# Optimization experiments

Hardware: AMD Instinct MI355X
Metric: run time of the kernel (lower is better)

The kernel has to match this reference:

```python
import jax, jax.numpy as jnp
import numpy as np

B, H, W, C = 32, 128, 128, 64
MX, MY = 32, 32  # modes_x, modes_y


def setup_inputs() -> dict:
    key = jax.random.key(0)
    k1, k2, k3, k4 = jax.random.split(key, 4)
    # glorot-ish scales for the spectral and conv weights
    wscale = (2.0 / (C + C)) ** 0.5
    return {
        "x": jax.random.normal(k1, (B, H, W, C), dtype=jnp.float32),
        "w_real": jax.random.normal(k2, (MX, MY, C, C), dtype=jnp.float32) * wscale,
        "w_imag": jax.random.normal(k3, (MX, MY, C, C), dtype=jnp.float32) * wscale,
        "conv_w": jax.random.normal(k4, (C, C), dtype=jnp.float32) * wscale,
        "conv_b": jnp.zeros((C,), dtype=jnp.float32),
    }


def reference(x, w_real, w_imag, conv_w, conv_b):
    # Complex spectral mixing weights [MX, MY, Cin, Cout]
    weights = jax.lax.complex(w_real, w_imag)
    # tf.signal.fft2d transforms the innermost TWO axes of [B,H,W,C],
    # i.e. axes (W, C); jnp.fft.fft2 default axes=(-2,-1) matches exactly.
    x_ft = jnp.fft.fft2(x.astype(jnp.complex64))           # [B,H,W,C] complex64
    # Mode truncation on axes (H, W), as in the original code.
    x_ft_trunc = x_ft[:, :MX, :MY, :]                      # [B,MX,MY,C]
    # Complex channel-mixing einsum over the low modes.
    x_ft_proc = jnp.einsum('bxyi,xyio->bxyo', x_ft_trunc, weights)  # [B,MX,MY,C]
    # Zero-pad back to the full grid on (H, W).
    x_ft_padded = jnp.pad(x_ft_proc,
                          ((0, 0), (0, H - MX), (0, W - MY), (0, 0)))
    # IFFT again over innermost two axes (W, C), take real part.
    x_spec = jnp.real(jnp.fft.ifft2(x_ft_padded))          # [B,H,W,C] float32
    # 1x1 conv (pointwise channel mix) + bias on the raw input.
    x_local = jnp.einsum('bhwi,io->bhwo', x, conv_w) + conv_b
    return jax.nn.relu(x_spec + x_local)
```

## Files before the change

kernel.cpp:

```cpp
#include <hip/hip_runtime.h>

typedef __attribute__((ext_vector_type(8))) short short8;
typedef __attribute__((ext_vector_type(4))) short bf16x4;
typedef __attribute__((ext_vector_type(4))) float f32x4;
typedef unsigned short ushort_t;

#define MFMA(a, b, c) __builtin_amdgcn_mfma_f32_16x16x32_bf16((a), (b), (c), 0, 0, 0)

constexpr int NB = 32, NHt = 128, NWd = 128, NC = 64, MX = 32;
constexpr float TWO_PI = 6.28318530717958647692f;

constexpr size_t TAB_T3 = 32768;
constexpr size_t TAB_T4 = 49152;
constexpr size_t XY_OFF = 65536;

__device__ inline ushort_t f2bf(float f) {
    union { float f; unsigned int u; } v; v.f = f;
    unsigned int r = v.u + 0x7FFFu + ((v.u >> 16) & 1u);
    return (ushort_t)(r >> 16);
}
__device__ inline int sxor(int row) { return ((row >> 3) & 3) << 4; }

__global__ __launch_bounds__(512) void k1_fwd(
    const float* __restrict__ x, char* __restrict__ tabs, ushort_t* __restrict__ XY)
{
    const int b = blockIdx.x, h = blockIdx.y;
    const int tid = threadIdx.x, lane = tid & 63, wv = tid >> 6;
    constexpr int SXT  = 0;
    constexpr int M1RE = 17408;
    constexpr int M1IM = 17408 + 4608;
    __shared__ __align__(16) char sm[26624];

    if (b == 0 && h == 0) {
        {
            int nt2 = tid >> 7, ks2 = (tid >> 6) & 1, l = tid & 63;
            int cc2 = (l & 15) + 16 * nt2, ob = (l >> 4) * 8 + 32 * ks2;
            short8 vre, vim;
            #pragma unroll
            for (int j = 0; j < 8; ++j) {
                float a = (float)(((ob + j) * cc2) & 63) * (TWO_PI / 64.f);
                float s, c; __sincosf(a, &s, &c);
                vre[j] = (short)f2bf(c); vim[j] = (short)f2bf(s);
            }
            *reinterpret_cast<short8*>(tabs + TAB_T3 + tid * 32)      = vre;
            *reinterpret_cast<short8*>(tabs + TAB_T3 + tid * 32 + 16) = vim;
        }
        {
            int mt2 = tid >> 6, l = tid & 63;
            int w = (l & 15) + 16 * mt2, ub = (l >> 4) * 8;
            short8 vre, vim;
            #pragma unroll
            for (int j = 0; j < 8; ++j) {
                float a = (float)((w * (ub + j)) & 127) * (TWO_PI / 128.f);
                float s, c; __sincosf(a, &s, &c);
                vre[j] = (short)f2bf(c * 0.0001220703125f);
                vim[j] = (short)f2bf(s * 0.0001220703125f);
            }
            *reinterpret_cast<short8*>(tabs + TAB_T4 + tid * 32)      = vre;
            *reinterpret_cast<short8*>(tabs + TAB_T4 + tid * 32 + 16) = vim;
        }
    }

    const float* xs = x + ((size_t)(b * NHt + h)) * (NWd * NC);
    #pragma unroll
    for (int i = 0; i < 4; ++i) {
        int idx = tid + 512 * i;
        int w = idx >> 4, c4 = (idx & 15) * 4;
        f32x4 v = *reinterpret_cast<const f32x4*>(xs + w * 64 + c4);
        #pragma unroll
        for (int j = 0; j < 4; ++j)
            *(ushort_t*)(sm + SXT + (c4 + j) * 272 + ((w * 2) ^ sxor(c4 + j))) = f2bf(v[j]);
    }
    __syncthreads();

    const int mt = wv >> 2, nt = wv & 3;
    f32x4 m1r = {0.f,0.f,0.f,0.f}, m1i = {0.f,0.f,0.f,0.f};
    const int cc = (lane & 15) + 16 * nt;
    const int uu = (lane & 15) + 16 * mt;
    #pragma unroll
    for (int ks = 0; ks < 4; ++ks) {
        short8 bfrag = *reinterpret_cast<const short8*>(
            sm + SXT + cc * 272 + (((lane >> 4) * 16 + 64 * ks) ^ sxor(cc)));
        int wb = (lane >> 4) * 8 + 32 * ks;
        short8 are, aim;
        #pragma unroll
        for (int j = 0; j < 8; ++j) {
            float a = (float)((uu * (wb + j)) & 127) * (TWO_PI / 128.f);
            float s, c; __sincosf(a, &s, &c);
            are[j] = (short)f2bf(c); aim[j] = (short)f2bf(-s);
        }
        m1r = MFMA(are, bfrag, m1r);
        m1i = MFMA(aim, bfrag, m1i);
    }
    #pragma unroll
    for (int r = 0; r < 4; ++r) {
        int u = (lane >> 4) * 4 + r + 16 * mt;
        int c = (lane & 15) + 16 * nt;
        *(ushort_t*)(sm + M1RE + u * 144 + c * 2) = f2bf(m1r[r]);
        *(ushort_t*)(sm + M1IM + u * 144 + c * 2) = f2bf(m1i[r]);
    }
    __syncthreads();

    f32x4 xP = {0.f,0.f,0.f,0.f}, xQ = {0.f,0.f,0.f,0.f}, xI = {0.f,0.f,0.f,0.f};
    const int kk = (lane & 15) + 16 * nt;
    #pragma unroll
    for (int ks = 0; ks < 2; ++ks) {
        short8 are = *reinterpret_cast<const short8*>(
            sm + M1RE + ((lane & 15) + 16 * mt) * 144 + (lane >> 4) * 16 + 64 * ks);
        short8 aim = *reinterpret_cast<const short8*>(
            sm + M1IM + ((lane & 15) + 16 * mt) * 144 + (lane >> 4) * 16 + 64 * ks);
        int cb2 = (lane >> 4) * 8 + 32 * ks;
        short8 bre, bim;
        #pragma unroll
        for (int j = 0; j < 8; ++j) {
            float a = (float)((kk * (cb2 + j)) & 63) * (TWO_PI / 64.f);
            float s, c; __sincosf(a, &s, &c);
            bre[j] = (short)f2bf(c); bim[j] = (short)f2bf(-s);
        }
        xP = MFMA(are, bre, xP);
        xQ = MFMA(aim, bim, xQ);
        xI = MFMA(are, bim, xI);
        xI = MFMA(aim, bre, xI);
    }
    #pragma unroll
    for (int r = 0; r < 4; ++r) {
        int u = (lane >> 4) * 4 + r + 16 * mt;
        int k = (lane & 15) + 16 * nt;
        *(ushort_t*)(sm + SXT + 0    + u * 128 + k * 2) = f2bf(xP[r] - xQ[r]);
        *(ushort_t*)(sm + SXT + 4096 + u * 128 + k * 2) = f2bf(xI[r]);
    }
    __syncthreads();

    {
        int u = tid >> 4, comp = (tid >> 3) & 1, k8 = (tid & 7) * 8;
        short8 v = *reinterpret_cast<const short8*>(sm + SXT + comp * 4096 + u * 128 + k8 * 2);
        size_t hu = (size_t)(h * 32 + u);
        *reinterpret_cast<short8*>(XY + ((hu * 2 + comp) * 32 + b) * 64 + k8) = v;
    }
}

__global__ __launch_bounds__(256) void k2_mix(
    const float* __restrict__ wre, const float* __restrict__ wim, ushort_t* __restrict__ XY)
{
    const int h = blockIdx.x, u = blockIdx.y;
    const int tid = threadIdx.x, lane = tid & 63, wv = tid >> 6;
    constexpr int XRE = 0, XIM = 4608, WTR = 9216, WTI = 18432;
    __shared__ __align__(16) char sm[27648];
    const size_t hu = (size_t)(h * 32 + u);

    #pragma unroll
    for (int it = 0; it < 2; ++it) {
        int row = (tid >> 3) + 32 * it;
        int comp = row >> 5, bb = row & 31, k8 = (tid & 7) * 8;
        short8 v = *reinterpret_cast<const short8*>(XY + ((hu * 2 + comp) * 32 + bb) * 64 + k8);
        *reinterpret_cast<short8*>(sm + (comp ? XIM : XRE) + bb * 144 + k8 * 2) = v;
    }
    const float* wr = wre + hu * 4096;
    const float* wi = wim + hu * 4096;
    #pragma unroll
    for (int i = 0; i < 4; ++i) {
        int idx = tid + 256 * i;
        int k = idx >> 4, o4 = (idx & 15) * 4;
        f32x4 vr = __builtin_nontemporal_load(reinterpret_cast<const f32x4*>(wr + k * 64 + o4));
        f32x4 vi = __builtin_nontemporal_load(reinterpret_cast<const f32x4*>(wi + k * 64 + o4));
        #pragma unroll
        for (int j = 0; j < 4; ++j) {
            int o = o4 + j, koff = (k * 2) ^ sxor(o);
            *(ushort_t*)(sm + WTR + o * 144 + koff) = f2bf(vr[j]);
            *(ushort_t*)(sm + WTI + o * 144 + koff) = f2bf(vi[j]);
        }
    }
    __syncthreads();

    const int mt = wv >> 1;
    f32x4 yRe[2], yIm[2];
    #pragma unroll
    for (int half = 0; half < 2; ++half) {
        const int nt = (wv & 1) * 2 + half;
        const int oo = (lane & 15) + 16 * nt;
        f32x4 yP = {0.f,0.f,0.f,0.f}, yQ = {0.f,0.f,0.f,0.f}, yI = {0.f,0.f,0.f,0.f};
        #pragma unroll
        for (int ks = 0; ks < 2; ++ks) {
            int woff = ((lane >> 4) * 16 + 64 * ks) ^ sxor(oo);
            short8 are = *reinterpret_cast<const short8*>(
                sm + XRE + ((lane & 15) + 16 * mt) * 144 + (lane >> 4) * 16 + 64 * ks);
            short8 aim = *reinterpret_cast<const short8*>(
                sm + XIM + ((lane & 15) + 16 * mt) * 144 + (lane >> 4) * 16 + 64 * ks);
            short8 bre = *reinterpret_cast<const short8*>(sm + WTR + oo * 144 + woff);
            short8 bim = *reinterpret_cast<const short8*>(sm + WTI + oo * 144 + woff);
            yP = MFMA(are, bre, yP); yQ = MFMA(aim, bim, yQ);
            yI = MFMA(are, bim, yI); yI = MFMA(aim, bre, yI);
        }
        #pragma unroll
        for (int r = 0; r < 4; ++r) { yRe[half][r] = yP[r] - yQ[r]; yIm[half][r] = yI[r]; }
    }
    __syncthreads();

    #pragma unroll
    for (int half = 0; half < 2; ++half) {
        const int nt = (wv & 1) * 2 + half;
        #pragma unroll
        for (int r = 0; r < 4; ++r) {
            int bb = (lane >> 4) * 4 + r + 16 * mt;
            int o = (lane & 15) + 16 * nt;
            *(ushort_t*)(sm + 0    + bb * 128 + o * 2) = f2bf(yRe[half][r]);
            *(ushort_t*)(sm + 4096 + bb * 128 + o * 2) = f2bf(yIm[half][r]);
        }
    }
    __syncthreads();

    #pragma unroll
    for (int it = 0; it < 2; ++it) {
        int flat = tid + 256 * it;
        short8 v = *reinterpret_cast<const short8*>(sm + flat * 16);
        *reinterpret_cast<short8*>(XY + hu * 4096 + flat * 8) = v;
    }
}

__global__ __launch_bounds__(512, 4) void k3_inv(
    const float* __restrict__ x, const float* __restrict__ cw, const float* __restrict__ cb,
    const char* __restrict__ tabs, const ushort_t* __restrict__ XY, float* __restrict__ out)
{
    const int b = blockIdx.x, h = blockIdx.y;
    const int tid = threadIdx.x, lane = tid & 63, wv = tid >> 6;
    constexpr int ST_RE = 0, ST_IM = 5120;
    constexpr int XB   = 10240;
    constexpr int CWT  = 28672;
    constexpr int SCB  = 37888;
    constexpr int OUTB = 38144;
    constexpr int YRE  = 38144;
    constexpr int YIM  = 38144 + 4608;
    __shared__ __align__(16) char sm[72960];

    const float* xs = x + ((size_t)(b * NHt + h)) * (NWd * NC);
    f32x4 xv[4];
    #pragma unroll
    for (int i = 0; i < 4; ++i) {
        int idx = tid + 512 * i;
        int w = idx >> 4, c4 = (idx & 15) * 4;
        xv[i] = __builtin_nontemporal_load(reinterpret_cast<const f32x4*>(xs + w * 64 + c4));
    }
    short8 yv = {}, gre = {}, gim = {};
    if (h < MX) {
        int u = tid >> 4, comp = (tid >> 3) & 1, o8 = (tid & 7) * 8;
        size_t hu = (size_t)(h * 32 + u);
        yv = *reinterpret_cast<const short8*>(XY + ((hu * 2 + comp) * 32 + b) * 64 + o8);
        const char* t4 = tabs + TAB_T4 + ((wv * 64 + lane) * 32);
        gre = *reinterpret_cast<const short8*>(t4);
        gim = *reinterpret_cast<const short8*>(t4 + 16);
    }

    #pragma unroll
    for (int i = 0; i < 4; ++i) {
        int idx = tid + 512 * i;
        int w = idx >> 4, c4 = (idx & 15) * 4;
        bf16x4 pk = { (short)f2bf(xv[i][0]), (short)f2bf(xv[i][1]),
                      (short)f2bf(xv[i][2]), (short)f2bf(xv[i][3]) };
        *reinterpret_cast<bf16x4*>(sm + XB + w * 144 + c4 * 2) = pk;
    }
    #pragma unroll
    for (int i = 0; i < 2; ++i) {
        int ii = (tid >> 4) + 32 * i;
        #pragma unroll
        for (int j = 0; j < 4; ++j) {
            int o = (tid & 15) + 16 * j;
            *(ushort_t*)(sm + CWT + o * 144 + ii * 2) = f2bf(cw[ii * 64 + o]);
        }
    }
    if (tid < 64) ((float*)(sm + SCB))[tid] = cb[tid];

    if (h < MX) {
        {
            int u = tid >> 4, comp = (tid >> 3) & 1, o8 = (tid & 7) * 8;
            *reinterpret_cast<short8*>(sm + (comp ? YIM : YRE) + u * 144 + o8 * 2) = yv;
        }
        __syncthreads();
        const int mt = wv >> 2, nt = wv & 3;
        f32x4 sP = {0.f,0.f,0.f,0.f}, sQ = {0.f,0.f,0.f,0.f}, sI = {0.f,0.f,0.f,0.f};
        #pragma unroll
        for (int ks = 0; ks < 2; ++ks) {
            short8 are = *reinterpret_cast<const short8*>(
                sm + YRE + ((lane & 15) + 16 * mt) * 144 + (lane >> 4) * 16 + 64 * ks);
            short8 aim = *reinterpret_cast<const short8*>(
                sm + YIM + ((lane & 15) + 16 * mt) * 144 + (lane >> 4) * 16 + 64 * ks);
            const char* t3 = tabs + TAB_T3 + (((nt * 2 + ks) * 64 + lane) * 32);
            short8 bre = *reinterpret_cast<const short8*>(t3);
            short8 bim = *reinterpret_cast<const short8*>(t3 + 16);
            sP = MFMA(are, bre, sP); sQ = MFMA(aim, bim, sQ);
            sI = MFMA(are, bim, sI); sI = MFMA(aim, bre, sI);
        }
        #pragma unroll
        for (int r = 0; r < 4; ++r) {
            int u = (lane >> 4) * 4 + r + 16 * mt;
            int c = (lane & 15) + 16 * nt;
            *(ushort_t*)(sm + ST_RE + c * 80 + u * 2) = f2bf(sP[r] - sQ[r]);
            *(ushort_t*)(sm + ST_IM + c * 80 + u * 2) = f2bf(sI[r]);
        }
    }
    __syncthreads();

    #pragma unroll
    for (int nt = 0; nt < 4; ++nt) {
        f32x4 acc = {0.f,0.f,0.f,0.f};
        #pragma unroll
        for (int ks = 0; ks < 2; ++ks) {
            short8 ah = *reinterpret_cast<const short8*>(
                sm + XB + ((lane & 15) + 16 * wv) * 144 + (lane >> 4) * 16 + 64 * ks);
            short8 bw = *reinterpret_cast<const short8*>(
                sm + CWT + ((lane & 15) + 16 * nt) * 144 + (lane >> 4) * 16 + 64 * ks);
            acc = MFMA(ah, bw, acc);
        }
        f32x4 sp = {0.f,0.f,0.f,0.f}, sq = {0.f,0.f,0.f,0.f};
        if (h < MX) {
            short8 bre = *reinterpret_cast<const short8*>(
                sm + ST_RE + ((lane & 15) + 16 * nt) * 80 + (lane >> 4) * 16);
            short8 bim = *reinterpret_cast<const short8*>(
                sm + ST_IM + ((lane & 15) + 16 * nt) * 80 + (lane >> 4) * 16);
            sp = MFMA(gre, bre, sp);
            sq = MFMA(gim, bim, sq);
        }
        #pragma unroll
        for (int r = 0; r < 4; ++r) {
            int w = (lane >> 4) * 4 + r + 16 * wv;
            int c = (lane & 15) + 16 * nt;
            float v = acc[r] + ((const float*)(sm + SCB))[c];
            if (h < MX) v += sp[r] - sq[r];
            *(float*)(sm + OUTB + w * 272 + c * 4) = fmaxf(v, 0.0f);
        }
    }
    __syncthreads();

    float* orow = out + ((size_t)(b * NHt + h)) * (NWd * NC);
    #pragma unroll
    for (int i = 0; i < 4; ++i) {
        int flat = tid + 512 * i;
        int w = flat >> 4, c4 = (flat & 15) * 4;
        f32x4 v = *reinterpret_cast<const f32x4*>(sm + OUTB + w * 272 + c4 * 4);
        __builtin_nontemporal_store(v, reinterpret_cast<f32x4*>(orow + w * 64 + c4));
    }
}

extern "C" void kernel_launch(void* const* d_in, const int* in_sizes, int n_in,
                              void* d_out, int out_size, void* d_ws, size_t ws_size,
                              hipStream_t stream) {
    const float* x      = (const float*)d_in[0];
    const float* w_real = (const float*)d_in[1];
    const float* w_imag = (const float*)d_in[2];
    const float* conv_w = (const float*)d_in[3];
    const float* conv_b = (const float*)d_in[4];
    float* out = (float*)d_out;

    char* tabs   = (char*)d_ws;
    ushort_t* XY = (ushort_t*)((char*)d_ws + XY_OFF);

    k1_fwd<<<dim3(NB, MX), 512, 0, stream>>>(x, tabs, XY);
    k2_mix<<<dim3(MX, 32), 256, 0, stream>>>(w_real, w_imag, XY);
    k3_inv<<<dim3(NB, NHt), 512, 0, stream>>>(x, conv_w, conv_b,
                                              (const char*)tabs, XY, out);
}
```

Before: 84.48 us.

## Transpose inverse-kernel MFMAs to keep x in registers and store output directly

The inverse kernel now computes the output tile transposed (channels × width), so each lane's input x fragment is loaded straight from global memory into MFMA B-operand registers instead of being staged through LDS. The spectral and conv contributions accumulate into one accumulator, with the imaginary twiddle table pre-negated so the subtraction folds into MFMA accumulation. Results are written directly to global memory as float4 nontemporal stores, which removes the output LDS staging buffer and one barrier. Shared memory shrinks from about 73KB to 29KB and the launch bound occupancy hint rises to 6, at the cost of per-lane output stores that may be less coalesced.

Measured after the change: 94.97 us. +12.4%, slower.

```diff
diff --git a/kernel.cpp b/kernel.cpp
--- a/kernel.cpp
+++ b/kernel.cpp
@@ -46,15 +46,15 @@
             *reinterpret_cast<short8*>(tabs + TAB_T3 + tid * 32 + 16) = vim;
         }
         {
-            int mt2 = tid >> 6, l = tid & 63;
-            int w = (l & 15) + 16 * mt2, ub = (l >> 4) * 8;
+            int wt = tid >> 6, l = tid & 63;
+            int w = (l & 15) + 16 * wt, ub = (l >> 4) * 8;
             short8 vre, vim;
             #pragma unroll
             for (int j = 0; j < 8; ++j) {
                 float a = (float)((w * (ub + j)) & 127) * (TWO_PI / 128.f);
                 float s, c; __sincosf(a, &s, &c);
                 vre[j] = (short)f2bf(c * 0.0001220703125f);
-                vim[j] = (short)f2bf(s * 0.0001220703125f);
+                vim[j] = (short)f2bf(-s * 0.0001220703125f);
             }
             *reinterpret_cast<short8*>(tabs + TAB_T4 + tid * 32)      = vre;
             *reinterpret_cast<short8*>(tabs + TAB_T4 + tid * 32 + 16) = vim;
@@ -217,28 +217,26 @@
     }
 }
 
-__global__ __launch_bounds__(512, 4) void k3_inv(
+__global__ __launch_bounds__(512, 6) void k3_inv(
     const float* __restrict__ x, const float* __restrict__ cw, const float* __restrict__ cb,
     const char* __restrict__ tabs, const ushort_t* __restrict__ XY, float* __restrict__ out)
 {
     const int b = blockIdx.x, h = blockIdx.y;
     const int tid = threadIdx.x, lane = tid & 63, wv = tid >> 6;
-    constexpr int ST_RE = 0, ST_IM = 5120;
-    constexpr int XB   = 10240;
-    constexpr int CWT  = 28672;
-    constexpr int SCB  = 37888;
-    constexpr int OUTB = 38144;
-    constexpr int YRE  = 38144;
-    constexpr int YIM  = 38144 + 4608;
-    __shared__ __align__(16) char sm[72960];
+    constexpr int YRE   = 0, YIM = 4608;
+    constexpr int ST_RE = 9216, ST_IM = 14336;
+    constexpr int CWT   = 19456;
+    constexpr int SCB   = 28672;
+    __shared__ __align__(16) char sm[28928];
 
     const float* xs = x + ((size_t)(b * NHt + h)) * (NWd * NC);
-    f32x4 xv[4];
-    #pragma unroll
-    for (int i = 0; i < 4; ++i) {
-        int idx = tid + 512 * i;
-        int w = idx >> 4, c4 = (idx & 15) * 4;
-        xv[i] = __builtin_nontemporal_load(reinterpret_cast<const f32x4*>(xs + w * 64 + c4));
+    const int ww = (lane & 15) + 16 * wv;
+    const float* xrow = xs + ww * 64 + (lane >> 4) * 8;
+    f32x4 xa[4];
+    #pragma unroll
+    for (int ks = 0; ks < 2; ++ks) {
+        xa[2*ks]   = __builtin_nontemporal_load(reinterpret_cast<const f32x4*>(xrow + 32 * ks));
+        xa[2*ks+1] = __builtin_nontemporal_load(reinterpret_cast<const f32x4*>(xrow + 32 * ks + 4));
     }
     short8 yv = {}, gre = {}, gim = {};
     if (h < MX) {
@@ -251,14 +249,6 @@
     }
 
     #pragma unroll
-    for (int i = 0; i < 4; ++i) {
-        int idx = tid + 512 * i;
-        int w = idx >> 4, c4 = (idx & 15) * 4;
-        bf16x4 pk = { (short)f2bf(xv[i][0]), (short)f2bf(xv[i][1]),
-                      (short)f2bf(xv[i][2]), (short)f2bf(xv[i][3]) };
-        *reinterpret_cast<bf16x4*>(sm + XB + w * 144 + c4 * 2) = pk;
-    }
-    #pragma unroll
     for (int i = 0; i < 2; ++i) {
         int ii = (tid >> 4) + 32 * i;
         #pragma unroll
@@ -269,12 +259,24 @@
     }
     if (tid < 64) ((float*)(sm + SCB))[tid] = cb[tid];
 
+    short8 xb[2];
+    #pragma unroll
+    for (int ks = 0; ks < 2; ++ks) {
+        short8 t;
+        #pragma unroll
+        for (int j = 0; j < 4; ++j) {
+            t[j]     = (short)f2bf(xa[2*ks][j]);
+            t[4 + j] = (short)f2bf(xa[2*ks+1][j]);
+        }
+        xb[ks] = t;
+    }
     if (h < MX) {
-        {
-            int u = tid >> 4, comp = (tid >> 3) & 1, o8 = (tid & 7) * 8;
-            *reinterpret_cast<short8*>(sm + (comp ? YIM : YRE) + u * 144 + o8 * 2) = yv;
-        }
-        __syncthreads();
+        int u = tid >> 4, comp = (tid >> 3) & 1, o8 = (tid & 7) * 8;
+        *reinterpret_cast<short8*>(sm + (comp ? YIM : YRE) + u * 144 + o8 * 2) = yv;
+    }
+    __syncthreads();
+
+    if (h < MX) {
         const int mt = wv >> 2, nt = wv & 3;
         f32x4 sP = {0.f,0.f,0.f,0.f}, sQ = {0.f,0.f,0.f,0.f}, sI = {0.f,0.f,0.f,0.f};
         #pragma unroll
@@ -296,47 +298,33 @@
             *(ushort_t*)(sm + ST_RE + c * 80 + u * 2) = f2bf(sP[r] - sQ[r]);
             *(ushort_t*)(sm + ST_IM + c * 80 + u * 2) = f2bf(sI[r]);
         }
-    }
-    __syncthreads();
-
-    #pragma unroll
-    for (int nt = 0; nt < 4; ++nt) {
+        __syncthreads();
+    }
+
+    float* orow = out + ((size_t)(b * NHt + h)) * (NWd * NC);
+    #pragma unroll
+    for (int mt = 0; mt < 4; ++mt) {
         f32x4 acc = {0.f,0.f,0.f,0.f};
         #pragma unroll
         for (int ks = 0; ks < 2; ++ks) {
-            short8 ah = *reinterpret_cast<const short8*>(
-                sm + XB + ((lane & 15) + 16 * wv) * 144 + (lane >> 4) * 16 + 64 * ks);
-            short8 bw = *reinterpret_cast<const short8*>(
-                sm + CWT + ((lane & 15) + 16 * nt) * 144 + (lane >> 4) * 16 + 64 * ks);
-            acc = MFMA(ah, bw, acc);
-        }
-        f32x4 sp = {0.f,0.f,0.f,0.f}, sq = {0.f,0.f,0.f,0.f};
+            short8 aw = *reinterpret_cast<const short8*>(
+                sm + CWT + ((lane & 15) + 16 * mt) * 144 + (lane >> 4) * 16 + 64 * ks);
+            acc = MFMA(aw, xb[ks], acc);
+        }
         if (h < MX) {
-            short8 bre = *reinterpret_cast<const short8*>(
-                sm + ST_RE + ((lane & 15) + 16 * nt) * 80 + (lane >> 4) * 16);
-            short8 bim = *reinterpret_cast<const short8*>(
-                sm + ST_IM + ((lane & 15) + 16 * nt) * 80 + (lane >> 4) * 16);
-            sp = MFMA(gre, bre, sp);
-            sq = MFMA(gim, bim, sq);
-        }
-        #pragma unroll
-        for (int r = 0; r < 4; ++r) {
-            int w = (lane >> 4) * 4 + r + 16 * wv;
-            int c = (lane & 15) + 16 * nt;
-            float v = acc[r] + ((const float*)(sm + SCB))[c];
-            if (h < MX) v += sp[r] - sq[r];
-            *(float*)(sm + OUTB + w * 272 + c * 4) = fmaxf(v, 0.0f);
-        }
-    }
-    __syncthreads();
-
-    float* orow = out + ((size_t)(b * NHt + h)) * (NWd * NC);
-    #pragma unroll
-    for (int i = 0; i < 4; ++i) {
-        int flat = tid + 512 * i;
-        int w = flat >> 4, c4 = (flat & 15) * 4;
-        f32x4 v = *reinterpret_cast<const f32x4*>(sm + OUTB + w * 272 + c4 * 4);
-        __builtin_nontemporal_store(v, reinterpret_cast<f32x4*>(orow + w * 64 + c4));
+            short8 sre = *reinterpret_cast<const short8*>(
+                sm + ST_RE + ((lane & 15) + 16 * mt) * 80 + (lane >> 4) * 16);
+            short8 sim = *reinterpret_cast<const short8*>(
+                sm + ST_IM + ((lane & 15) + 16 * mt) * 80 + (lane >> 4) * 16);
+            acc = MFMA(sre, gre, acc);
+            acc = MFMA(sim, gim, acc);
+        }
+        int obase = (lane >> 4) * 4 + 16 * mt;
+        f32x4 bias = *reinterpret_cast<const f32x4*>(sm + SCB + obase * 4);
+        f32x4 v;
+        #pragma unroll
+        for (int r = 0; r < 4; ++r) v[r] = fmaxf(acc[r] + bias[r], 0.0f);
+        __builtin_nontemporal_store(v, reinterpret_cast<f32x4*>(orow + ww * 64 + obase));
     }
 }
 
```

## Move non-spectral rows' pointwise conv into mix kernel; restrict inverse to low rows

Applied to the files above, without the earlier changes.

Rows h >= MX have no spectral contribution, so their 1x1 conv + bias + relu is now computed by extra blocks appended to the spectral-mixing kernel, in 64-wide half-row tiles. The inverse kernel is launched only over the MX low rows and drops its h<MX branches. This overlaps the bulk of the output bandwidth with the small mixing work and cuts the inverse kernel's grid. The mixed kernel now has heterogeneous blocks that share one shared-memory size, and the conv blocks compete with mixing blocks for compute units.

Measured after the change: 76.76 us. 1.1x faster.

```diff
diff --git a/kernel.cpp b/kernel.cpp
--- a/kernel.cpp
+++ b/kernel.cpp
@@ -139,85 +139,152 @@
     }
 }
 
-__global__ __launch_bounds__(256) void k2_mix(
-    const float* __restrict__ wre, const float* __restrict__ wim, ushort_t* __restrict__ XY)
+__global__ __launch_bounds__(256) void k2_fused(
+    const float* __restrict__ wre, const float* __restrict__ wim,
+    ushort_t* __restrict__ XY,
+    const float* __restrict__ x, const float* __restrict__ cw,
+    const float* __restrict__ cb, float* __restrict__ out)
 {
-    const int h = blockIdx.x, u = blockIdx.y;
+    const int bid = blockIdx.x;
     const int tid = threadIdx.x, lane = tid & 63, wv = tid >> 6;
-    constexpr int XRE = 0, XIM = 4608, WTR = 9216, WTI = 18432;
-    __shared__ __align__(16) char sm[27648];
-    const size_t hu = (size_t)(h * 32 + u);
-
-    #pragma unroll
-    for (int it = 0; it < 2; ++it) {
-        int row = (tid >> 3) + 32 * it;
-        int comp = row >> 5, bb = row & 31, k8 = (tid & 7) * 8;
-        short8 v = *reinterpret_cast<const short8*>(XY + ((hu * 2 + comp) * 32 + bb) * 64 + k8);
-        *reinterpret_cast<short8*>(sm + (comp ? XIM : XRE) + bb * 144 + k8 * 2) = v;
-    }
-    const float* wr = wre + hu * 4096;
-    const float* wi = wim + hu * 4096;
-    #pragma unroll
-    for (int i = 0; i < 4; ++i) {
-        int idx = tid + 256 * i;
-        int k = idx >> 4, o4 = (idx & 15) * 4;
-        f32x4 vr = __builtin_nontemporal_load(reinterpret_cast<const f32x4*>(wr + k * 64 + o4));
-        f32x4 vi = __builtin_nontemporal_load(reinterpret_cast<const f32x4*>(wi + k * 64 + o4));
-        #pragma unroll
-        for (int j = 0; j < 4; ++j) {
-            int o = o4 + j, koff = (k * 2) ^ sxor(o);
-            *(ushort_t*)(sm + WTR + o * 144 + koff) = f2bf(vr[j]);
-            *(ushort_t*)(sm + WTI + o * 144 + koff) = f2bf(vi[j]);
-        }
-    }
-    __syncthreads();
-
-    const int mt = wv >> 1;
-    f32x4 yRe[2], yIm[2];
-    #pragma unroll
-    for (int half = 0; half < 2; ++half) {
-        const int nt = (wv & 1) * 2 + half;
-        const int oo = (lane & 15) + 16 * nt;
-        f32x4 yP = {0.f,0.f,0.f,0.f}, yQ = {0.f,0.f,0.f,0.f}, yI = {0.f,0.f,0.f,0.f};
-        #pragma unroll
-        for (int ks = 0; ks < 2; ++ks) {
-            int woff = ((lane >> 4) * 16 + 64 * ks) ^ sxor(oo);
-            short8 are = *reinterpret_cast<const short8*>(
-                sm + XRE + ((lane & 15) + 16 * mt) * 144 + (lane >> 4) * 16 + 64 * ks);
-            short8 aim = *reinterpret_cast<const short8*>(
-                sm + XIM + ((lane & 15) + 16 * mt) * 144 + (lane >> 4) * 16 + 64 * ks);
-            short8 bre = *reinterpret_cast<const short8*>(sm + WTR + oo * 144 + woff);
-            short8 bim = *reinterpret_cast<const short8*>(sm + WTI + oo * 144 + woff);
-            yP = MFMA(are, bre, yP); yQ = MFMA(aim, bim, yQ);
-            yI = MFMA(are, bim, yI); yI = MFMA(aim, bre, yI);
-        }
-        #pragma unroll
-        for (int r = 0; r < 4; ++r) { yRe[half][r] = yP[r] - yQ[r]; yIm[half][r] = yI[r]; }
-    }
-    __syncthreads();
-
-    #pragma unroll
-    for (int half = 0; half < 2; ++half) {
-        const int nt = (wv & 1) * 2 + half;
-        #pragma unroll
-        for (int r = 0; r < 4; ++r) {
-            int bb = (lane >> 4) * 4 + r + 16 * mt;
-            int o = (lane & 15) + 16 * nt;
-            *(ushort_t*)(sm + 0    + bb * 128 + o * 2) = f2bf(yRe[half][r]);
-            *(ushort_t*)(sm + 4096 + bb * 128 + o * 2) = f2bf(yIm[half][r]);
-        }
-    }
-    __syncthreads();
-
-    #pragma unroll
-    for (int it = 0; it < 2; ++it) {
-        int flat = tid + 256 * it;
-        short8 v = *reinterpret_cast<const short8*>(sm + flat * 16);
-        *reinterpret_cast<short8*>(XY + hu * 4096 + flat * 8) = v;
+    __shared__ __align__(16) char sm[36096];
+
+    if (bid < 1024) {
+        const int h = bid >> 5, u = bid & 31;
+        constexpr int XRE = 0, XIM = 4608, WTR = 9216, WTI = 18432;
+        const size_t hu = (size_t)(h * 32 + u);
+
+        #pragma unroll
+        for (int it = 0; it < 2; ++it) {
+            int row = (tid >> 3) + 32 * it;
+            int comp = row >> 5, bb = row & 31, k8 = (tid & 7) * 8;
+            short8 v = *reinterpret_cast<const short8*>(XY + ((hu * 2 + comp) * 32 + bb) * 64 + k8);
+            *reinterpret_cast<short8*>(sm + (comp ? XIM : XRE) + bb * 144 + k8 * 2) = v;
+        }
+        const float* wr = wre + hu * 4096;
+        const float* wi = wim + hu * 4096;
+        #pragma unroll
+        for (int i = 0; i < 4; ++i) {
+            int idx = tid + 256 * i;
+            int k = idx >> 4, o4 = (idx & 15) * 4;
+            f32x4 vr = __builtin_nontemporal_load(reinterpret_cast<const f32x4*>(wr + k * 64 + o4));
+            f32x4 vi = __builtin_nontemporal_load(reinterpret_cast<const f32x4*>(wi + k * 64 + o4));
+            #pragma unroll
+            for (int j = 0; j < 4; ++j) {
+                int o = o4 + j, koff = (k * 2) ^ sxor(o);
+                *(ushort_t*)(sm + WTR + o * 144 + koff) = f2bf(vr[j]);
+                *(ushort_t*)(sm + WTI + o * 144 + koff) = f2bf(vi[j]);
+            }
+        }
+        __syncthreads();
+
+        const int mt = wv >> 1;
+        f32x4 yRe[2], yIm[2];
+        #pragma unroll
+        for (int half = 0; half < 2; ++half) {
+            const int nt = (wv & 1) * 2 + half;
+            const int oo = (lane & 15) + 16 * nt;
+            f32x4 yP = {0.f,0.f,0.f,0.f}, yQ = {0.f,0.f,0.f,0.f}, yI = {0.f,0.f,0.f,0.f};
+            #pragma unroll
+            for (int ks = 0; ks < 2; ++ks) {
+                int woff = ((lane >> 4) * 16 + 64 * ks) ^ sxor(oo);
+                short8 are = *reinterpret_cast<const short8*>(
+                    sm + XRE + ((lane & 15) + 16 * mt) * 144 + (lane >> 4) * 16 + 64 * ks);
+                short8 aim = *reinterpret_cast<const short8*>(
+                    sm + XIM + ((lane & 15) + 16 * mt) * 144 + (lane >> 4) * 16 + 64 * ks);
+                short8 bre = *reinterpret_cast<const short8*>(sm + WTR + oo * 144 + woff);
+                short8 bim = *reinterpret_cast<const short8*>(sm + WTI + oo * 144 + woff);
+                yP = MFMA(are, bre, yP); yQ = MFMA(aim, bim, yQ);
+                yI = MFMA(are, bim, yI); yI = MFMA(aim, bre, yI);
+            }
+            #pragma unroll
+            for (int r = 0; r < 4; ++r) { yRe[half][r] = yP[r] - yQ[r]; yIm[half][r] = yI[r]; }
+        }
+        __syncthreads();
+
+        #pragma unroll
+        for (int half = 0; half < 2; ++half) {
+            const int nt = (wv & 1) * 2 + half;
+            #pragma unroll
+            for (int r = 0; r < 4; ++r) {
+                int bb = (lane >> 4) * 4 + r + 16 * mt;
+                int o = (lane & 15) + 16 * nt;
+                *(ushort_t*)(sm + 0    + bb * 128 + o * 2) = f2bf(yRe[half][r]);
+                *(ushort_t*)(sm + 4096 + bb * 128 + o * 2) = f2bf(yIm[half][r]);
+            }
+        }
+        __syncthreads();
+
+        #pragma unroll
+        for (int it = 0; it < 2; ++it) {
+            int flat = tid + 256 * it;
+            short8 v = *reinterpret_cast<const short8*>(sm + flat * 16);
+            *reinterpret_cast<short8*>(XY + hu * 4096 + flat * 8) = v;
+        }
+    } else {
+        const int cid = bid - 1024;
+        const int b = cid / 192, rem = cid % 192;
+        const int h = MX + (rem >> 1), w0 = (rem & 1) * 64;
+        constexpr int XB   = 0;
+        constexpr int CWT  = 9216;
+        constexpr int SCB  = 18432;
+        constexpr int OUTB = 18688;
+
+        const float* xs = x + (((size_t)(b * NHt + h)) * NWd + w0) * NC;
+        #pragma unroll
+        for (int i = 0; i < 4; ++i) {
+            int idx = tid + 256 * i;
+            int w = idx >> 4, c4 = (idx & 15) * 4;
+            f32x4 v = *reinterpret_cast<const f32x4*>(xs + w * 64 + c4);
+            bf16x4 pk = { (short)f2bf(v[0]), (short)f2bf(v[1]),
+                          (short)f2bf(v[2]), (short)f2bf(v[3]) };
+            *reinterpret_cast<bf16x4*>(sm + XB + w * 144 + c4 * 2) = pk;
+        }
+        #pragma unroll
+        for (int i = 0; i < 4; ++i) {
+            int ii = (tid >> 4) + 16 * i;
+            #pragma unroll
+            for (int j = 0; j < 4; ++j) {
+                int o = (tid & 15) + 16 * j;
+                *(ushort_t*)(sm + CWT + o * 144 + ii * 2) = f2bf(cw[ii * 64 + o]);
+            }
+        }
+        if (tid < 64) ((float*)(sm + SCB))[tid] = cb[tid];
+        __syncthreads();
+
+        #pragma unroll
+        for (int nt = 0; nt < 4; ++nt) {
+            f32x4 acc = {0.f,0.f,0.f,0.f};
+            #pragma unroll
+            for (int ks = 0; ks < 2; ++ks) {
+                short8 ah = *reinterpret_cast<const short8*>(
+                    sm + XB + ((lane & 15) + 16 * wv) * 144 + (lane >> 4) * 16 + 64 * ks);
+                short8 bw = *reinterpret_cast<const short8*>(
+                    sm + CWT + ((lane & 15) + 16 * nt) * 144 + (lane >> 4) * 16 + 64 * ks);
+                acc = MFMA(ah, bw, acc);
+            }
+            #pragma unroll
+            for (int r = 0; r < 4; ++r) {
+                int w = (lane >> 4) * 4 + r + 16 * wv;
+                int c = (lane & 15) + 16 * nt;
+                float v = acc[r] + ((const float*)(sm + SCB))[c];
+                *(float*)(sm + OUTB + w * 272 + c * 4) = fmaxf(v, 0.0f);
+            }
+        }
+        __syncthreads();
+
+        float* orow = out + (((size_t)(b * NHt + h)) * NWd + w0) * NC;
+        #pragma unroll
+        for (int i = 0; i < 4; ++i) {
+            int flat = tid + 256 * i;
+            int w = flat >> 4, c4 = (flat & 15) * 4;
+            f32x4 v = *reinterpret_cast<const f32x4*>(sm + OUTB + w * 272 + c4 * 4);
+            __builtin_nontemporal_store(v, reinterpret_cast<f32x4*>(orow + w * 64 + c4));
+        }
     }
 }
 
-__global__ __launch_bounds__(512, 4) void k3_inv(
+__global__ __launch_bounds__(512, 4) void k3_spec(
     const float* __restrict__ x, const float* __restrict__ cw, const float* __restrict__ cb,
     const char* __restrict__ tabs, const ushort_t* __restrict__ XY, float* __restrict__ out)
 {
@@ -240,8 +307,8 @@
         int w = idx >> 4, c4 = (idx & 15) * 4;
         xv[i] = __builtin_nontemporal_load(reinterpret_cast<const f32x4*>(xs + w * 64 + c4));
     }
-    short8 yv = {}, gre = {}, gim = {};
-    if (h < MX) {
+    short8 yv, gre, gim;
+    {
         int u = tid >> 4, comp = (tid >> 3) & 1, o8 = (tid & 7) * 8;
         size_t hu = (size_t)(h * 32 + u);
         yv = *reinterpret_cast<const short8*>(XY + ((hu * 2 + comp) * 32 + b) * 64 + o8);
@@ -268,13 +335,13 @@
         }
     }
     if (tid < 64) ((float*)(sm + SCB))[tid] = cb[tid];
-
-    if (h < MX) {
-        {
-            int u = tid >> 4, comp = (tid >> 3) & 1, o8 = (tid & 7) * 8;
-            *reinterpret_cast<short8*>(sm + (comp ? YIM : YRE) + u * 144 + o8 * 2) = yv;
-        }
-        __syncthreads();
+    {
+        int u = tid >> 4, comp = (tid >> 3) & 1, o8 = (tid & 7) * 8;
+        *reinterpret_cast<short8*>(sm + (comp ? YIM : YRE) + u * 144 + o8 * 2) = yv;
+    }
+    __syncthreads();
+
+    {
         const int mt = wv >> 2, nt = wv & 3;
         f32x4 sP = {0.f,0.f,0.f,0.f}, sQ = {0.f,0.f,0.f,0.f}, sI = {0.f,0.f,0.f,0.f};
         #pragma unroll
@@ -310,21 +377,18 @@
                 sm + CWT + ((lane & 15) + 16 * nt) * 144 + (lane >> 4) * 16 + 64 * ks);
             acc = MFMA(ah, bw, acc);
         }
+        short8 bre = *reinterpret_cast<const short8*>(
+            sm + ST_RE + ((lane & 15) + 16 * nt) * 80 + (lane >> 4) * 16);
+        short8 bim = *reinterpret_cast<const short8*>(
+            sm + ST_IM + ((lane & 15) + 16 * nt) * 80 + (lane >> 4) * 16);
         f32x4 sp = {0.f,0.f,0.f,0.f}, sq = {0.f,0.f,0.f,0.f};
-        if (h < MX) {
-            short8 bre = *reinterpret_cast<const short8*>(
-                sm + ST_RE + ((lane & 15) + 16 * nt) * 80 + (lane >> 4) * 16);
-            short8 bim = *reinterpret_cast<const short8*>(
-                sm + ST_IM + ((lane & 15) + 16 * nt) * 80 + (lane >> 4) * 16);
-            sp = MFMA(gre, bre, sp);
-            sq = MFMA(gim, bim, sq);
-        }
+        sp = MFMA(gre, bre, sp);
+        sq = MFMA(gim, bim, sq);
         #pragma unroll
         for (int r = 0; r < 4; ++r) {
             int w = (lane >> 4) * 4 + r + 16 * wv;
             int c = (lane & 15) + 16 * nt;
-            float v = acc[r] + ((const float*)(sm + SCB))[c];
-            if (h < MX) v += sp[r] - sq[r];
+            float v = acc[r] + ((const float*)(sm + SCB))[c] + sp[r] - sq[r];
             *(float*)(sm + OUTB + w * 272 + c * 4) = fmaxf(v, 0.0f);
         }
     }
@@ -354,7 +418,8 @@
     ushort_t* XY = (ushort_t*)((char*)d_ws + XY_OFF);
 
     k1_fwd<<<dim3(NB, MX), 512, 0, stream>>>(x, tabs, XY);
-    k2_mix<<<dim3(MX, 32), 256, 0, stream>>>(w_real, w_imag, XY);
-    k3_inv<<<dim3(NB, NHt), 512, 0, stream>>>(x, conv_w, conv_b,
+    k2_fused<<<1024 + NB * (NHt - MX) * 2, 256, 0, stream>>>(
+        w_real, w_imag, XY, x, conv_w, conv_b, out);
+    k3_spec<<<dim3(NB, MX), 512, 0, stream>>>(x, conv_w, conv_b,
                                               (const char*)tabs, XY, out);
 }
```
